# Kernel tuning notes

Measured on AMD Instinct MI355X. Metric: run time of the kernel, lower is better.

Reference implementation:

```python
import jax, jax.numpy as jnp
import numpy as np

B, L, E = 4096, 50, 128


def setup_inputs() -> dict:
    key = jax.random.key(0)
    ks = jax.random.split(key, 12)
    s = 1.0 / np.sqrt(E)
    return {
        "A": jax.random.uniform(ks[0], (B, L, 2 * L), dtype=jnp.float32),
        "hidden": jax.random.normal(ks[1], (B, L, E), dtype=jnp.float32),
        "w_ih": jax.random.normal(ks[2], (3 * E, 2 * E), dtype=jnp.float32) * s,
        "w_hh": jax.random.normal(ks[3], (3 * E, E), dtype=jnp.float32) * s,
        "b_ih": jax.random.normal(ks[4], (3 * E,), dtype=jnp.float32) * s,
        "b_hh": jax.random.normal(ks[5], (3 * E,), dtype=jnp.float32) * s,
        "b_iah": jax.random.normal(ks[6], (E,), dtype=jnp.float32) * s,
        "b_ioh": jax.random.normal(ks[7], (E,), dtype=jnp.float32) * s,
        "w_in": jax.random.normal(ks[8], (E, E), dtype=jnp.float32) * s,
        "b_in": jax.random.normal(ks[9], (E,), dtype=jnp.float32) * s,
        "w_out": jax.random.normal(ks[10], (E, E), dtype=jnp.float32) * s,
        "b_out": jax.random.normal(ks[11], (E,), dtype=jnp.float32) * s,
    }


STEP = 1


def _gnn_cell(A, hidden, w_ih, w_hh, b_ih, b_hh, b_iah, b_ioh, w_in, b_in, w_out, b_out):
    L_ = A.shape[1]
    # linear_edge_in / linear_edge_out (torch Linear: x @ W.T + b)
    h_in = jnp.einsum('ble,fe->blf', hidden, w_in) + b_in
    h_out = jnp.einsum('ble,fe->blf', hidden, w_out) + b_out
    # adjacency propagation: A = [A_in | A_out] along last dim
    input_in = jnp.matmul(A[:, :, :L_], h_in) + b_iah     # [B,L,E]
    input_out = jnp.matmul(A[:, :, L_:2 * L_], h_out) + b_ioh
    inputs = jnp.concatenate([input_in, input_out], axis=2)  # [B,L,2E]
    gi = jnp.einsum('blf,gf->blg', inputs, w_ih) + b_ih      # [B,L,3E]
    gh = jnp.einsum('ble,ge->blg', hidden, w_hh) + b_hh      # [B,L,3E]
    i_r, i_i, i_n = jnp.split(gi, 3, axis=2)
    h_r, h_i, h_n = jnp.split(gh, 3, axis=2)
    reset_gate = jax.nn.sigmoid(i_r + h_r)
    input_gate = jax.nn.sigmoid(i_i + h_i)
    new_gate = jnp.tanh(i_n + reset_gate * h_n)
    return (1 - input_gate) * hidden + input_gate * new_gate


def reference(A, hidden, w_ih, w_hh, b_ih, b_hh, b_iah, b_ioh, w_in, b_in, w_out, b_out):
    for _ in range(STEP):
        hidden = _gnn_cell(A, hidden, w_ih, w_hh, b_ih, b_hh, b_iah, b_ioh, w_in, b_in, w_out, b_out)
    return hidden
```

## Files before the change

kernel.cpp:

```cpp
#include <hip/hip_runtime.h>


using f32x4 = __attribute__((ext_vector_type(4))) float;
using s16x8 = __attribute__((ext_vector_type(8))) short;
using u32x2 = __attribute__((ext_vector_type(2))) unsigned;

#define MFMA(a, b, c) __builtin_amdgcn_mfma_f32_16x16x32_bf16((a), (b), (c), 0, 0, 0)

__device__ __forceinline__ unsigned short f2bf(float x) {
    unsigned u = __float_as_uint(x);
    u += 0x7fffu + ((u >> 16) & 1u);
    return (unsigned short)(u >> 16);
}
__device__ __forceinline__ float bf2f(unsigned short b) {
    return __uint_as_float(((unsigned)b) << 16);
}
__device__ __forceinline__ unsigned pkbf(float a, float b) {
    unsigned r;
    asm("v_cvt_pk_bf16_f32 %0, %1, %2" : "=v"(r) : "v"(a), "v"(b));
    return r;
}

__global__ void wconv_kernel(const float* __restrict__ w_in, const float* __restrict__ w_out,
                             const float* __restrict__ w_hh, const float* __restrict__ w_ih,
                             unsigned short* __restrict__ W1, unsigned short* __restrict__ Wih) {
    int i = blockIdx.x * 256 + threadIdx.x;
    if (i < 81920) {
        float v = (i < 16384) ? w_in[i] : (i < 32768) ? w_out[i - 16384] : w_hh[i - 32768];
        W1[i] = f2bf(v);
    } else if (i < 180224) {
        int j = i - 81920;
        Wih[j] = f2bf(w_ih[j]);
    }
}

#define LDS_BYTES 125952

__launch_bounds__(512, 1)
__global__ void gnn_kernel(const float* __restrict__ A, const float* __restrict__ H,
                           const unsigned short* __restrict__ W1, const unsigned short* __restrict__ Wih,
                           const float* __restrict__ b_ih, const float* __restrict__ b_hh,
                           const float* __restrict__ b_iah, const float* __restrict__ b_ioh,
                           const float* __restrict__ b_in, const float* __restrict__ b_out,
                           float* __restrict__ out) {
    extern __shared__ char smem[];
    unsigned short* sHhi = (unsigned short*)(smem + 0);
    unsigned short* sHlo = (unsigned short*)(smem + 17408);
    unsigned short* sAhi = (unsigned short*)(smem + 34816);
    unsigned short* sThi = (unsigned short*)(smem + 52224);
    unsigned short* sTlo = (unsigned short*)(smem + 89088);
    unsigned short* sIhi = (unsigned short*)(smem + 52224);
    unsigned short* sIlo = (unsigned short*)(smem + 86016);

    const int b    = blockIdx.x;
    const int tid  = threadIdx.x;
    const int wv   = tid >> 6;
    const int lane = tid & 63;
    const int l16  = lane & 15;
    const int l4   = lane >> 4;

    const float* Hb = H + (size_t)b * 6400;
    const float* Ab = A + (size_t)b * 5000;

    s16x8 w1f[4][5];
    #pragma unroll
    for (int kt = 0; kt < 4; ++kt)
        #pragma unroll
        for (int t = 0; t < 5; ++t)
            w1f[kt][t] = *(const s16x8*)(W1 + ((wv + 8 * t) * 16 + l16) * 128 + kt * 32 + l4 * 8);

    {
        const float4* H4 = (const float4*)Hb;
        #pragma unroll
        for (int i = 0; i < 4; ++i) {
            int idx = i * 512 + tid;
            if (idx < 1600) {
                int r = idx >> 5, c = (idx & 31) * 4;
                float4 v = H4[idx];
                unsigned h01 = pkbf(v.x, v.y), h23 = pkbf(v.z, v.w);
                float g0 = __uint_as_float(h01 << 16), g1 = __uint_as_float(h01 & 0xffff0000u);
                float g2 = __uint_as_float(h23 << 16), g3 = __uint_as_float(h23 & 0xffff0000u);
                unsigned l01 = pkbf(v.x - g0, v.y - g1), l23 = pkbf(v.z - g2, v.w - g3);
                u32x2 vh; vh[0] = h01; vh[1] = h23;
                u32x2 vl; vl[0] = l01; vl[1] = l23;
                *(u32x2*)(sHhi + r * 136 + c) = vh;
                *(u32x2*)(sHlo + r * 136 + c) = vl;
            }
        }
        #pragma unroll
        for (int i = 0; i < 4; ++i) {
            int idx = i * 512 + tid;
            if (idx < 1792) {
                int pl = idx >= 896 ? 1 : 0;
                int j = idx - pl * 896;
                int r = 50 + (j >> 6), c = (j & 63) * 2;
                *(unsigned*)((pl ? sHlo : sHhi) + r * 136 + c) = 0u;
            }
        }
        const float2* A2 = (const float2*)Ab;
        #pragma unroll
        for (int i = 0; i < 5; ++i) {
            int idx = i * 512 + tid;
            if (idx < 2500) {
                int r = idx / 50, j = idx - r * 50;
                float2 v = A2[idx];
                int dc = (j < 25) ? (2 * j) : (2 * j + 14);
                *(unsigned*)(sAhi + r * 136 + dc) = pkbf(v.x, v.y);
            }
        }
        #pragma unroll
        for (int i = 0; i < 4; ++i) {
            int idx = i * 512 + tid;
            if (idx < 1596) {
                int r, c;
                if (idx < 700) {
                    r = idx / 14; int k = idx - r * 14;
                    c = (k < 7) ? (50 + 2 * k) : (100 + 2 * k);
                } else {
                    int j = idx - 700;
                    r = 50 + (j >> 6); c = (j & 63) * 2;
                }
                *(unsigned*)(sAhi + r * 136 + c) = 0u;
            }
        }
    }
    __syncthreads();

    const f32x4 vzero = {0.f, 0.f, 0.f, 0.f};

    f32x4 acc_io[2][4];
    f32x4 acc_gh[3][4];
    #pragma unroll
    for (int t = 0; t < 2; ++t)
        #pragma unroll
        for (int m = 0; m < 4; ++m) acc_io[t][m] = vzero;
    #pragma unroll
    for (int t = 0; t < 3; ++t)
        #pragma unroll
        for (int m = 0; m < 4; ++m) acc_gh[t][m] = vzero;

    s16x8 ah[2][4], al[2][4];
    #pragma unroll
    for (int mt = 0; mt < 4; ++mt) {
        int off = (mt * 16 + l16) * 136 + l4 * 8;
        ah[0][mt] = *(const s16x8*)(sHhi + off);
        al[0][mt] = *(const s16x8*)(sHlo + off);
    }
    #pragma unroll
    for (int kt = 0; kt < 4; ++kt) {
        const int cur = kt & 1, nxt = cur ^ 1;
        if (kt < 3) {
            #pragma unroll
            for (int mt = 0; mt < 4; ++mt) {
                int off = (mt * 16 + l16) * 136 + (kt + 1) * 32 + l4 * 8;
                ah[nxt][mt] = *(const s16x8*)(sHhi + off);
                al[nxt][mt] = *(const s16x8*)(sHlo + off);
            }
        }
        #pragma unroll
        for (int t = 0; t < 5; ++t)
            #pragma unroll
            for (int mt = 0; mt < 4; ++mt) {
                if (t < 2) {
                    f32x4 a = acc_io[t][mt];
                    a = MFMA(ah[cur][mt], w1f[kt][t], a);
                    a = MFMA(al[cur][mt], w1f[kt][t], a);
                    acc_io[t][mt] = a;
                } else {
                    f32x4 a = acc_gh[t - 2][mt];
                    a = MFMA(ah[cur][mt], w1f[kt][t], a);
                    a = MFMA(al[cur][mt], w1f[kt][t], a);
                    acc_gh[t - 2][mt] = a;
                }
            }
    }

    s16x8 wihf[8][3];
    #pragma unroll
    for (int kt = 0; kt < 8; ++kt)
        #pragma unroll
        for (int t = 0; t < 3; ++t)
            wihf[kt][t] = *(const s16x8*)(Wih + ((wv + 8 * t) * 16 + l16) * 256 + kt * 32 + l4 * 8);

    #pragma unroll
    for (int t = 0; t < 2; ++t) {
        int n = (wv + 8 * t) * 16 + l16;
        float bias = (n < 128) ? b_in[n] : b_out[n - 128];
        #pragma unroll
        for (int mt = 0; mt < 4; ++mt) {
            int mb = mt * 16 + l4 * 4;
            float x0 = acc_io[t][mt][0] + bias, x1 = acc_io[t][mt][1] + bias;
            float x2 = acc_io[t][mt][2] + bias, x3 = acc_io[t][mt][3] + bias;
            unsigned h01 = pkbf(x0, x1), h23 = pkbf(x2, x3);
            float g0 = __uint_as_float(h01 << 16), g1 = __uint_as_float(h01 & 0xffff0000u);
            float g2 = __uint_as_float(h23 << 16), g3 = __uint_as_float(h23 & 0xffff0000u);
            unsigned l01 = pkbf(x0 - g0, x1 - g1), l23 = pkbf(x2 - g2, x3 - g3);
            u32x2 vh; vh[0] = h01; vh[1] = h23;
            u32x2 vl; vl[0] = l01; vl[1] = l23;
            *(u32x2*)(sThi + n * 72 + mb) = vh;
            *(u32x2*)(sTlo + n * 72 + mb) = vl;
        }
    }
    __syncthreads();

    const int p = wv >> 2, q = wv & 3;
    f32x4 acc2[2][4];
    #pragma unroll
    for (int t = 0; t < 2; ++t)
        #pragma unroll
        for (int m = 0; m < 4; ++m) acc2[t][m] = vzero;

    {
        s16x8 a2[2][4], th2[2][2], tl2[2][2];
        #pragma unroll
        for (int kt = 0; kt < 2; ++kt) {
            #pragma unroll
            for (int mt = 0; mt < 4; ++mt)
                a2[kt][mt] = *(const s16x8*)(sAhi + (mt * 16 + l16) * 136 + p * 64 + kt * 32 + l4 * 8);
            #pragma unroll
            for (int t = 0; t < 2; ++t) {
                int hr = p * 128 + (q + 4 * t) * 16 + l16;
                th2[kt][t] = *(const s16x8*)(sThi + hr * 72 + kt * 32 + l4 * 8);
                tl2[kt][t] = *(const s16x8*)(sTlo + hr * 72 + kt * 32 + l4 * 8);
            }
        }
        #pragma unroll
        for (int kt = 0; kt < 2; ++kt)
            #pragma unroll
            for (int t = 0; t < 2; ++t)
                #pragma unroll
                for (int mt = 0; mt < 4; ++mt) {
                    f32x4 a = acc2[t][mt];
                    a = MFMA(a2[kt][mt], th2[kt][t], a);
                    a = MFMA(a2[kt][mt], tl2[kt][t], a);
                    acc2[t][mt] = a;
                }
    }
    __syncthreads();
    #pragma unroll
    for (int t = 0; t < 2; ++t) {
        int n = p * 128 + (q + 4 * t) * 16 + l16;
        float bias = (n < 128) ? b_iah[n] : b_ioh[n - 128];
        #pragma unroll
        for (int mt = 0; mt < 4; ++mt) {
            int mb = mt * 16 + l4 * 4;
            #pragma unroll
            for (int rr = 0; rr < 4; rr += 2) {
                float x0 = acc2[t][mt][rr] + bias, x1 = acc2[t][mt][rr + 1] + bias;
                unsigned h = pkbf(x0, x1);
                float g0 = __uint_as_float(h << 16), g1 = __uint_as_float(h & 0xffff0000u);
                unsigned l = pkbf(x0 - g0, x1 - g1);
                sIhi[(mb + rr) * 264 + n]     = (unsigned short)(h & 0xffffu);
                sIhi[(mb + rr + 1) * 264 + n] = (unsigned short)(h >> 16);
                sIlo[(mb + rr) * 264 + n]     = (unsigned short)(l & 0xffffu);
                sIlo[(mb + rr + 1) * 264 + n] = (unsigned short)(l >> 16);
            }
        }
    }
    __syncthreads();

    f32x4 acc_n[4];
    #pragma unroll
    for (int m = 0; m < 4; ++m) acc_n[m] = vzero;

    #pragma unroll
    for (int mt = 0; mt < 4; ++mt) {
        int off = (mt * 16 + l16) * 264 + l4 * 8;
        ah[0][mt] = *(const s16x8*)(sIhi + off);
        al[0][mt] = *(const s16x8*)(sIlo + off);
    }
    #pragma unroll
    for (int kt = 0; kt < 8; ++kt) {
        const int cur = kt & 1, nxt = cur ^ 1;
        if (kt < 7) {
            #pragma unroll
            for (int mt = 0; mt < 4; ++mt) {
                int off = (mt * 16 + l16) * 264 + (kt + 1) * 32 + l4 * 8;
                ah[nxt][mt] = *(const s16x8*)(sIhi + off);
                al[nxt][mt] = *(const s16x8*)(sIlo + off);
            }
        }
        #pragma unroll
        for (int t = 0; t < 3; ++t)
            #pragma unroll
            for (int mt = 0; mt < 4; ++mt) {
                if (t < 2) {
                    f32x4 a = acc_gh[t][mt];
                    a = MFMA(ah[cur][mt], wihf[kt][t], a);
                    a = MFMA(al[cur][mt], wihf[kt][t], a);
                    acc_gh[t][mt] = a;
                } else {
                    f32x4 a = acc_n[mt];
                    a = MFMA(ah[cur][mt], wihf[kt][t], a);
                    a = MFMA(al[cur][mt], wihf[kt][t], a);
                    acc_n[mt] = a;
                }
            }
    }

    {
        const int e = wv * 16 + l16;
        const float br   = b_ih[e]       + b_hh[e];
        const float bi   = b_ih[128 + e] + b_hh[128 + e];
        const float bn_i = b_ih[256 + e];
        const float bn_h = b_hh[256 + e];
        float* Ob = out + (size_t)b * 6400;
        #pragma unroll
        for (int mt = 0; mt < 4; ++mt) {
            #pragma unroll
            for (int r = 0; r < 4; ++r) {
                int m = mt * 16 + l4 * 4 + r;
                if (m < 50) {
                    float argr = acc_gh[0][mt][r] + br;
                    float argi = acc_gh[1][mt][r] + bi;
                    float i_n  = acc_n[mt][r] + bn_i;
                    float h_n  = acc_gh[2][mt][r] + bn_h;
                    float rg = 1.f / (1.f + __expf(-argr));
                    float ig = 1.f / (1.f + __expf(-argi));
                    float ta = i_n + rg * h_n;
                    ta = fminf(fmaxf(ta, -30.f), 30.f);
                    float ex = __expf(2.f * ta);
                    float ng = (ex - 1.f) / (ex + 1.f);
                    float h0 = bf2f(sHhi[m * 136 + e]) + bf2f(sHlo[m * 136 + e]);
                    Ob[m * 128 + e] = h0 + ig * (ng - h0);
                }
            }
        }
    }
}

extern "C" void kernel_launch(void* const* d_in, const int* in_sizes, int n_in,
                              void* d_out, int out_size, void* d_ws, size_t ws_size,
                              hipStream_t stream) {
    const float* A     = (const float*)d_in[0];
    const float* hidden= (const float*)d_in[1];
    const float* w_ih  = (const float*)d_in[2];
    const float* w_hh  = (const float*)d_in[3];
    const float* b_ih  = (const float*)d_in[4];
    const float* b_hh  = (const float*)d_in[5];
    const float* b_iah = (const float*)d_in[6];
    const float* b_ioh = (const float*)d_in[7];
    const float* w_in  = (const float*)d_in[8];
    const float* b_in  = (const float*)d_in[9];
    const float* w_out = (const float*)d_in[10];
    const float* b_out = (const float*)d_in[11];
    float* out = (float*)d_out;

    unsigned short* W1  = (unsigned short*)d_ws;
    unsigned short* Wih = W1 + 81920;

    wconv_kernel<<<704, 256, 0, stream>>>(w_in, w_out, w_hh, w_ih, W1, Wih);

    const int nbatch = in_sizes[1] / 6400;
    (void)hipFuncSetAttribute((const void*)gnn_kernel,
                              hipFuncAttributeMaxDynamicSharedMemorySize, LDS_BYTES);
    gnn_kernel<<<nbatch, 512, LDS_BYTES, stream>>>(A, hidden, W1, Wih,
                                                   b_ih, b_hh, b_iah, b_ioh,
                                                   b_in, b_out, out);
}
```

Before: 542.4 us.

## Make blocks persistent over 16 batches with register prefetch of next inputs

Each block now loops over 16 consecutive batch elements instead of handling one. The LDS padding zeroing is done once per block. The next element's H and A are loaded into registers while the current one is computed, so global load latency overlaps with MFMA work. The cost is that the grid shrinks from 4096 to 256 blocks, which roughly matches the CU count at one block per CU, so per-CU latency hiding now depends on the prefetch. Weight fragments are still reloaded every iteration, and the extra prefetch registers raise register pressure.

```diff
diff --git a/kernel.cpp b/kernel.cpp
--- a/kernel.cpp
+++ b/kernel.cpp
@@ -3,6 +3,7 @@
 
 using f32x4 = __attribute__((ext_vector_type(4))) float;
 using s16x8 = __attribute__((ext_vector_type(8))) short;
+using s16x4 = __attribute__((ext_vector_type(4))) short;
 using u32x2 = __attribute__((ext_vector_type(2))) unsigned;
 
 #define MFMA(a, b, c) __builtin_amdgcn_mfma_f32_16x16x32_bf16((a), (b), (c), 0, 0, 0)
@@ -42,7 +43,7 @@
                            const float* __restrict__ b_ih, const float* __restrict__ b_hh,
                            const float* __restrict__ b_iah, const float* __restrict__ b_ioh,
                            const float* __restrict__ b_in, const float* __restrict__ b_out,
-                           float* __restrict__ out) {
+                           float* __restrict__ out, int nbatch) {
     extern __shared__ char smem[];
     unsigned short* sHhi = (unsigned short*)(smem + 0);
     unsigned short* sHlo = (unsigned short*)(smem + 17408);
@@ -52,35 +53,75 @@
     unsigned short* sIhi = (unsigned short*)(smem + 52224);
     unsigned short* sIlo = (unsigned short*)(smem + 86016);
 
-    const int b    = blockIdx.x;
     const int tid  = threadIdx.x;
     const int wv   = tid >> 6;
     const int lane = tid & 63;
     const int l16  = lane & 15;
     const int l4   = lane >> 4;
 
-    const float* Hb = H + (size_t)b * 6400;
-    const float* Ab = A + (size_t)b * 5000;
-
-    s16x8 w1f[4][5];
     #pragma unroll
-    for (int kt = 0; kt < 4; ++kt)
-        #pragma unroll
-        for (int t = 0; t < 5; ++t)
-            w1f[kt][t] = *(const s16x8*)(W1 + ((wv + 8 * t) * 16 + l16) * 128 + kt * 32 + l4 * 8);
-
+    for (int i = 0; i < 4; ++i) {
+        int idx = i * 512 + tid;
+        if (idx < 1792) {
+            int pl = idx >= 896 ? 1 : 0;
+            int j = idx - pl * 896;
+            int r = 50 + (j >> 6), c = (j & 63) * 2;
+            *(unsigned*)((pl ? sHlo : sHhi) + r * 136 + c) = 0u;
+        }
+    }
+    #pragma unroll
+    for (int i = 0; i < 4; ++i) {
+        int idx = i * 512 + tid;
+        if (idx < 1596) {
+            int r, c;
+            if (idx < 700) {
+                r = idx / 14; int k = idx - r * 14;
+                c = (k < 7) ? (50 + 2 * k) : (100 + 2 * k);
+            } else {
+                int j = idx - 700;
+                r = 50 + (j >> 6); c = (j & 63) * 2;
+            }
+            *(unsigned*)(sAhi + r * 136 + c) = 0u;
+        }
+    }
+
+    const int g0 = blockIdx.x * 16;
+    const int ng = (nbatch - g0 < 16) ? (nbatch - g0) : 16;
+
+    float4 hreg[4];
+    float2 areg[5];
     {
-        const float4* H4 = (const float4*)Hb;
+        const float4* H4 = (const float4*)(H + (size_t)g0 * 6400);
+        const float2* A2 = (const float2*)(A + (size_t)g0 * 5000);
+        #pragma unroll
+        for (int i = 0; i < 4; ++i) { int idx = i * 512 + tid; if (idx < 1600) hreg[i] = H4[idx]; }
+        #pragma unroll
+        for (int i = 0; i < 5; ++i) { int idx = i * 512 + tid; if (idx < 2500) areg[i] = A2[idx]; }
+    }
+
+    const f32x4 vzero = {0.f, 0.f, 0.f, 0.f};
+
+    #pragma unroll 1
+    for (int it = 0; it < ng; ++it) {
+        const int g = g0 + it;
+
+        s16x8 w1f[4][5];
+        #pragma unroll
+        for (int kt = 0; kt < 4; ++kt)
+            #pragma unroll
+            for (int t = 0; t < 5; ++t)
+                w1f[kt][t] = *(const s16x8*)(W1 + ((wv + 8 * t) * 16 + l16) * 128 + kt * 32 + l4 * 8);
+
         #pragma unroll
         for (int i = 0; i < 4; ++i) {
             int idx = i * 512 + tid;
             if (idx < 1600) {
                 int r = idx >> 5, c = (idx & 31) * 4;
-                float4 v = H4[idx];
+                float4 v = hreg[i];
                 unsigned h01 = pkbf(v.x, v.y), h23 = pkbf(v.z, v.w);
-                float g0 = __uint_as_float(h01 << 16), g1 = __uint_as_float(h01 & 0xffff0000u);
-                float g2 = __uint_as_float(h23 << 16), g3 = __uint_as_float(h23 & 0xffff0000u);
-                unsigned l01 = pkbf(v.x - g0, v.y - g1), l23 = pkbf(v.z - g2, v.w - g3);
+                float g0f = __uint_as_float(h01 << 16), g1f = __uint_as_float(h01 & 0xffff0000u);
+                float g2f = __uint_as_float(h23 << 16), g3f = __uint_as_float(h23 & 0xffff0000u);
+                unsigned l01 = pkbf(v.x - g0f, v.y - g1f), l23 = pkbf(v.z - g2f, v.w - g3f);
                 u32x2 vh; vh[0] = h01; vh[1] = h23;
                 u32x2 vl; vl[0] = l01; vl[1] = l23;
                 *(u32x2*)(sHhi + r * 136 + c) = vh;
@@ -88,244 +129,226 @@
             }
         }
         #pragma unroll
-        for (int i = 0; i < 4; ++i) {
-            int idx = i * 512 + tid;
-            if (idx < 1792) {
-                int pl = idx >= 896 ? 1 : 0;
-                int j = idx - pl * 896;
-                int r = 50 + (j >> 6), c = (j & 63) * 2;
-                *(unsigned*)((pl ? sHlo : sHhi) + r * 136 + c) = 0u;
-            }
-        }
-        const float2* A2 = (const float2*)Ab;
-        #pragma unroll
         for (int i = 0; i < 5; ++i) {
             int idx = i * 512 + tid;
             if (idx < 2500) {
                 int r = idx / 50, j = idx - r * 50;
-                float2 v = A2[idx];
+                float2 v = areg[i];
                 int dc = (j < 25) ? (2 * j) : (2 * j + 14);
                 *(unsigned*)(sAhi + r * 136 + dc) = pkbf(v.x, v.y);
             }
         }
-        #pragma unroll
-        for (int i = 0; i < 4; ++i) {
-            int idx = i * 512 + tid;
-            if (idx < 1596) {
-                int r, c;
-                if (idx < 700) {
-                    r = idx / 14; int k = idx - r * 14;
-                    c = (k < 7) ? (50 + 2 * k) : (100 + 2 * k);
-                } else {
-                    int j = idx - 700;
-                    r = 50 + (j >> 6); c = (j & 63) * 2;
-                }
-                *(unsigned*)(sAhi + r * 136 + c) = 0u;
-            }
-        }
-    }
-    __syncthreads();
-
-    const f32x4 vzero = {0.f, 0.f, 0.f, 0.f};
-
-    f32x4 acc_io[2][4];
-    f32x4 acc_gh[3][4];
-    #pragma unroll
-    for (int t = 0; t < 2; ++t)
-        #pragma unroll
-        for (int m = 0; m < 4; ++m) acc_io[t][m] = vzero;
-    #pragma unroll
-    for (int t = 0; t < 3; ++t)
-        #pragma unroll
-        for (int m = 0; m < 4; ++m) acc_gh[t][m] = vzero;
-
-    s16x8 ah[2][4], al[2][4];
-    #pragma unroll
-    for (int mt = 0; mt < 4; ++mt) {
-        int off = (mt * 16 + l16) * 136 + l4 * 8;
-        ah[0][mt] = *(const s16x8*)(sHhi + off);
-        al[0][mt] = *(const s16x8*)(sHlo + off);
-    }
-    #pragma unroll
-    for (int kt = 0; kt < 4; ++kt) {
-        const int cur = kt & 1, nxt = cur ^ 1;
-        if (kt < 3) {
+
+        if (it + 1 < ng) {
+            const float4* H4 = (const float4*)(H + (size_t)(g + 1) * 6400);
+            const float2* A2 = (const float2*)(A + (size_t)(g + 1) * 5000);
+            #pragma unroll
+            for (int i = 0; i < 4; ++i) { int idx = i * 512 + tid; if (idx < 1600) hreg[i] = H4[idx]; }
+            #pragma unroll
+            for (int i = 0; i < 5; ++i) { int idx = i * 512 + tid; if (idx < 2500) areg[i] = A2[idx]; }
+        }
+        __syncthreads();
+
+        f32x4 acc_io[2][4];
+        f32x4 acc_gh[3][4];
+        #pragma unroll
+        for (int t = 0; t < 2; ++t)
+            #pragma unroll
+            for (int m = 0; m < 4; ++m) acc_io[t][m] = vzero;
+        #pragma unroll
+        for (int t = 0; t < 3; ++t)
+            #pragma unroll
+            for (int m = 0; m < 4; ++m) acc_gh[t][m] = vzero;
+
+        s16x8 ah[2][4], al[2][4];
+        #pragma unroll
+        for (int mt = 0; mt < 4; ++mt) {
+            int off = (mt * 16 + l16) * 136 + l4 * 8;
+            ah[0][mt] = *(const s16x8*)(sHhi + off);
+            al[0][mt] = *(const s16x8*)(sHlo + off);
+        }
+        #pragma unroll
+        for (int kt = 0; kt < 4; ++kt) {
+            const int cur = kt & 1, nxt = cur ^ 1;
+            if (kt < 3) {
+                #pragma unroll
+                for (int mt = 0; mt < 4; ++mt) {
+                    int off = (mt * 16 + l16) * 136 + (kt + 1) * 32 + l4 * 8;
+                    ah[nxt][mt] = *(const s16x8*)(sHhi + off);
+                    al[nxt][mt] = *(const s16x8*)(sHlo + off);
+                }
+            }
+            #pragma unroll
+            for (int t = 0; t < 5; ++t)
+                #pragma unroll
+                for (int mt = 0; mt < 4; ++mt) {
+                    if (t < 2) {
+                        f32x4 a = acc_io[t][mt];
+                        a = MFMA(ah[cur][mt], w1f[kt][t], a);
+                        a = MFMA(al[cur][mt], w1f[kt][t], a);
+                        acc_io[t][mt] = a;
+                    } else {
+                        f32x4 a = acc_gh[t - 2][mt];
+                        a = MFMA(ah[cur][mt], w1f[kt][t], a);
+                        a = MFMA(al[cur][mt], w1f[kt][t], a);
+                        acc_gh[t - 2][mt] = a;
+                    }
+                }
+        }
+
+        s16x8 wihf[8][3];
+        #pragma unroll
+        for (int kt = 0; kt < 8; ++kt)
+            #pragma unroll
+            for (int t = 0; t < 3; ++t)
+                wihf[kt][t] = *(const s16x8*)(Wih + ((wv + 8 * t) * 16 + l16) * 256 + kt * 32 + l4 * 8);
+
+        #pragma unroll
+        for (int t = 0; t < 2; ++t) {
+            int n = (wv + 8 * t) * 16 + l16;
+            float bias = (n < 128) ? b_in[n] : b_out[n - 128];
             #pragma unroll
             for (int mt = 0; mt < 4; ++mt) {
-                int off = (mt * 16 + l16) * 136 + (kt + 1) * 32 + l4 * 8;
-                ah[nxt][mt] = *(const s16x8*)(sHhi + off);
-                al[nxt][mt] = *(const s16x8*)(sHlo + off);
-            }
-        }
-        #pragma unroll
-        for (int t = 0; t < 5; ++t)
+                int mb = mt * 16 + l4 * 4;
+                float x0 = acc_io[t][mt][0] + bias, x1 = acc_io[t][mt][1] + bias;
+                float x2 = acc_io[t][mt][2] + bias, x3 = acc_io[t][mt][3] + bias;
+                unsigned h01 = pkbf(x0, x1), h23 = pkbf(x2, x3);
+                float q0 = __uint_as_float(h01 << 16), q1 = __uint_as_float(h01 & 0xffff0000u);
+                float q2 = __uint_as_float(h23 << 16), q3 = __uint_as_float(h23 & 0xffff0000u);
+                unsigned l01 = pkbf(x0 - q0, x1 - q1), l23 = pkbf(x2 - q2, x3 - q3);
+                u32x2 vh; vh[0] = h01; vh[1] = h23;
+                u32x2 vl; vl[0] = l01; vl[1] = l23;
+                *(u32x2*)(sThi + n * 72 + mb) = vh;
+                *(u32x2*)(sTlo + n * 72 + mb) = vl;
+            }
+        }
+        __syncthreads();
+
+        const int p = wv >> 2, q = wv & 3;
+        f32x4 acc2[2][4];
+        #pragma unroll
+        for (int t = 0; t < 2; ++t)
+            #pragma unroll
+            for (int m = 0; m < 4; ++m) acc2[t][m] = vzero;
+
+        {
+            s16x8 a2[2][4], th2[2][2], tl2[2][2];
+            #pragma unroll
+            for (int kt = 0; kt < 2; ++kt) {
+                #pragma unroll
+                for (int mt = 0; mt < 4; ++mt)
+                    a2[kt][mt] = *(const s16x8*)(sAhi + (mt * 16 + l16) * 136 + p * 64 + kt * 32 + l4 * 8);
+                #pragma unroll
+                for (int t = 0; t < 2; ++t) {
+                    int hr = p * 128 + (q + 4 * t) * 16 + l16;
+                    th2[kt][t] = *(const s16x8*)(sThi + hr * 72 + kt * 32 + l4 * 8);
+                    tl2[kt][t] = *(const s16x8*)(sTlo + hr * 72 + kt * 32 + l4 * 8);
+                }
+            }
+            #pragma unroll
+            for (int kt = 0; kt < 2; ++kt)
+                #pragma unroll
+                for (int t = 0; t < 2; ++t)
+                    #pragma unroll
+                    for (int mt = 0; mt < 4; ++mt) {
+                        f32x4 a = acc2[t][mt];
+                        a = MFMA(a2[kt][mt], th2[kt][t], a);
+                        a = MFMA(a2[kt][mt], tl2[kt][t], a);
+                        acc2[t][mt] = a;
+                    }
+        }
+        __syncthreads();
+        #pragma unroll
+        for (int t = 0; t < 2; ++t) {
+            int n = p * 128 + (q + 4 * t) * 16 + l16;
+            float bias = (n < 128) ? b_iah[n] : b_ioh[n - 128];
             #pragma unroll
             for (int mt = 0; mt < 4; ++mt) {
-                if (t < 2) {
-                    f32x4 a = acc_io[t][mt];
-                    a = MFMA(ah[cur][mt], w1f[kt][t], a);
-                    a = MFMA(al[cur][mt], w1f[kt][t], a);
-                    acc_io[t][mt] = a;
-                } else {
-                    f32x4 a = acc_gh[t - 2][mt];
-                    a = MFMA(ah[cur][mt], w1f[kt][t], a);
-                    a = MFMA(al[cur][mt], w1f[kt][t], a);
-                    acc_gh[t - 2][mt] = a;
-                }
-            }
-    }
-
-    s16x8 wihf[8][3];
-    #pragma unroll
-    for (int kt = 0; kt < 8; ++kt)
-        #pragma unroll
-        for (int t = 0; t < 3; ++t)
-            wihf[kt][t] = *(const s16x8*)(Wih + ((wv + 8 * t) * 16 + l16) * 256 + kt * 32 + l4 * 8);
-
-    #pragma unroll
-    for (int t = 0; t < 2; ++t) {
-        int n = (wv + 8 * t) * 16 + l16;
-        float bias = (n < 128) ? b_in[n] : b_out[n - 128];
+                int mb = mt * 16 + l4 * 4;
+                #pragma unroll
+                for (int rr = 0; rr < 4; rr += 2) {
+                    float x0 = acc2[t][mt][rr] + bias, x1 = acc2[t][mt][rr + 1] + bias;
+                    unsigned h = pkbf(x0, x1);
+                    float q0 = __uint_as_float(h << 16), q1 = __uint_as_float(h & 0xffff0000u);
+                    unsigned l = pkbf(x0 - q0, x1 - q1);
+                    sIhi[(mb + rr) * 264 + n]     = (unsigned short)(h & 0xffffu);
+                    sIhi[(mb + rr + 1) * 264 + n] = (unsigned short)(h >> 16);
+                    sIlo[(mb + rr) * 264 + n]     = (unsigned short)(l & 0xffffu);
+                    sIlo[(mb + rr + 1) * 264 + n] = (unsigned short)(l >> 16);
+                }
+            }
+        }
+        __syncthreads();
+
+        f32x4 acc_n[4];
+        #pragma unroll
+        for (int m = 0; m < 4; ++m) acc_n[m] = vzero;
+
         #pragma unroll
         for (int mt = 0; mt < 4; ++mt) {
-            int mb = mt * 16 + l4 * 4;
-            float x0 = acc_io[t][mt][0] + bias, x1 = acc_io[t][mt][1] + bias;
-            float x2 = acc_io[t][mt][2] + bias, x3 = acc_io[t][mt][3] + bias;
-            unsigned h01 = pkbf(x0, x1), h23 = pkbf(x2, x3);
-            float g0 = __uint_as_float(h01 << 16), g1 = __uint_as_float(h01 & 0xffff0000u);
-            float g2 = __uint_as_float(h23 << 16), g3 = __uint_as_float(h23 & 0xffff0000u);
-            unsigned l01 = pkbf(x0 - g0, x1 - g1), l23 = pkbf(x2 - g2, x3 - g3);
-            u32x2 vh; vh[0] = h01; vh[1] = h23;
-            u32x2 vl; vl[0] = l01; vl[1] = l23;
-            *(u32x2*)(sThi + n * 72 + mb) = vh;
-            *(u32x2*)(sTlo + n * 72 + mb) = vl;
-        }
-    }
-    __syncthreads();
-
-    const int p = wv >> 2, q = wv & 3;
-    f32x4 acc2[2][4];
-    #pragma unroll
-    for (int t = 0; t < 2; ++t)
-        #pragma unroll
-        for (int m = 0; m < 4; ++m) acc2[t][m] = vzero;
-
-    {
-        s16x8 a2[2][4], th2[2][2], tl2[2][2];
-        #pragma unroll
-        for (int kt = 0; kt < 2; ++kt) {
-            #pragma unroll
-            for (int mt = 0; mt < 4; ++mt)
-                a2[kt][mt] = *(const s16x8*)(sAhi + (mt * 16 + l16) * 136 + p * 64 + kt * 32 + l4 * 8);
-            #pragma unroll
-            for (int t = 0; t < 2; ++t) {
-                int hr = p * 128 + (q + 4 * t) * 16 + l16;
-                th2[kt][t] = *(const s16x8*)(sThi + hr * 72 + kt * 32 + l4 * 8);
-                tl2[kt][t] = *(const s16x8*)(sTlo + hr * 72 + kt * 32 + l4 * 8);
-            }
-        }
-        #pragma unroll
-        for (int kt = 0; kt < 2; ++kt)
-            #pragma unroll
-            for (int t = 0; t < 2; ++t)
+            int off = (mt * 16 + l16) * 264 + l4 * 8;
+            ah[0][mt] = *(const s16x8*)(sIhi + off);
+            al[0][mt] = *(const s16x8*)(sIlo + off);
+        }
+        #pragma unroll
+        for (int kt = 0; kt < 8; ++kt) {
+            const int cur = kt & 1, nxt = cur ^ 1;
+            if (kt < 7) {
                 #pragma unroll
                 for (int mt = 0; mt < 4; ++mt) {
-                    f32x4 a = acc2[t][mt];
-                    a = MFMA(a2[kt][mt], th2[kt][t], a);
-                    a = MFMA(a2[kt][mt], tl2[kt][t], a);
-                    acc2[t][mt] = a;
-                }
-    }
-    __syncthreads();
-    #pragma unroll
-    for (int t = 0; t < 2; ++t) {
-        int n = p * 128 + (q + 4 * t) * 16 + l16;
-        float bias = (n < 128) ? b_iah[n] : b_ioh[n - 128];
-        #pragma unroll
-        for (int mt = 0; mt < 4; ++mt) {
-            int mb = mt * 16 + l4 * 4;
-            #pragma unroll
-            for (int rr = 0; rr < 4; rr += 2) {
-                float x0 = acc2[t][mt][rr] + bias, x1 = acc2[t][mt][rr + 1] + bias;
-                unsigned h = pkbf(x0, x1);
-                float g0 = __uint_as_float(h << 16), g1 = __uint_as_float(h & 0xffff0000u);
-                unsigned l = pkbf(x0 - g0, x1 - g1);
-                sIhi[(mb + rr) * 264 + n]     = (unsigned short)(h & 0xffffu);
-                sIhi[(mb + rr + 1) * 264 + n] = (unsigned short)(h >> 16);
-                sIlo[(mb + rr) * 264 + n]     = (unsigned short)(l & 0xffffu);
-                sIlo[(mb + rr + 1) * 264 + n] = (unsigned short)(l >> 16);
-            }
-        }
-    }
-    __syncthreads();
-
-    f32x4 acc_n[4];
-    #pragma unroll
-    for (int m = 0; m < 4; ++m) acc_n[m] = vzero;
-
-    #pragma unroll
-    for (int mt = 0; mt < 4; ++mt) {
-        int off = (mt * 16 + l16) * 264 + l4 * 8;
-        ah[0][mt] = *(const s16x8*)(sIhi + off);
-        al[0][mt] = *(const s16x8*)(sIlo + off);
-    }
-    #pragma unroll
-    for (int kt = 0; kt < 8; ++kt) {
-        const int cur = kt & 1, nxt = cur ^ 1;
-        if (kt < 7) {
+                    int off = (mt * 16 + l16) * 264 + (kt + 1) * 32 + l4 * 8;
+                    ah[nxt][mt] = *(const s16x8*)(sIhi + off);
+                    al[nxt][mt] = *(const s16x8*)(sIlo + off);
+                }
+            }
+            #pragma unroll
+            for (int t = 0; t < 3; ++t)
+                #pragma unroll
+                for (int mt = 0; mt < 4; ++mt) {
+                    if (t < 2) {
+                        f32x4 a = acc_gh[t][mt];
+                        a = MFMA(ah[cur][mt], wihf[kt][t], a);
+                        a = MFMA(al[cur][mt], wihf[kt][t], a);
+                        acc_gh[t][mt] = a;
+                    } else {
+                        f32x4 a = acc_n[mt];
+                        a = MFMA(ah[cur][mt], wihf[kt][t], a);
+                        a = MFMA(al[cur][mt], wihf[kt][t], a);
+                        acc_n[mt] = a;
+                    }
+                }
+        }
+
+        {
+            const int e = wv * 16 + l16;
+            const float br   = b_ih[e]       + b_hh[e];
+            const float bi   = b_ih[128 + e] + b_hh[128 + e];
+            const float bn_i = b_ih[256 + e];
+            const float bn_h = b_hh[256 + e];
+            float* Ob = out + (size_t)g * 6400;
             #pragma unroll
             for (int mt = 0; mt < 4; ++mt) {
-                int off = (mt * 16 + l16) * 264 + (kt + 1) * 32 + l4 * 8;
-                ah[nxt][mt] = *(const s16x8*)(sIhi + off);
-                al[nxt][mt] = *(const s16x8*)(sIlo + off);
-            }
-        }
-        #pragma unroll
-        for (int t = 0; t < 3; ++t)
-            #pragma unroll
-            for (int mt = 0; mt < 4; ++mt) {
-                if (t < 2) {
-                    f32x4 a = acc_gh[t][mt];
-                    a = MFMA(ah[cur][mt], wihf[kt][t], a);
-                    a = MFMA(al[cur][mt], wihf[kt][t], a);
-                    acc_gh[t][mt] = a;
-                } else {
-                    f32x4 a = acc_n[mt];
-                    a = MFMA(ah[cur][mt], wihf[kt][t], a);
-                    a = MFMA(al[cur][mt], wihf[kt][t], a);
-                    acc_n[mt] = a;
-                }
-            }
-    }
-
-    {
-        const int e = wv * 16 + l16;
-        const float br   = b_ih[e]       + b_hh[e];
-        const float bi   = b_ih[128 + e] + b_hh[128 + e];
-        const float bn_i = b_ih[256 + e];
-        const float bn_h = b_hh[256 + e];
-        float* Ob = out + (size_t)b * 6400;
-        #pragma unroll
-        for (int mt = 0; mt < 4; ++mt) {
-            #pragma unroll
-            for (int r = 0; r < 4; ++r) {
-                int m = mt * 16 + l4 * 4 + r;
-                if (m < 50) {
-                    float argr = acc_gh[0][mt][r] + br;
-                    float argi = acc_gh[1][mt][r] + bi;
-                    float i_n  = acc_n[mt][r] + bn_i;
-                    float h_n  = acc_gh[2][mt][r] + bn_h;
-                    float rg = 1.f / (1.f + __expf(-argr));
-                    float ig = 1.f / (1.f + __expf(-argi));
-                    float ta = i_n + rg * h_n;
-                    ta = fminf(fmaxf(ta, -30.f), 30.f);
-                    float ex = __expf(2.f * ta);
-                    float ng = (ex - 1.f) / (ex + 1.f);
-                    float h0 = bf2f(sHhi[m * 136 + e]) + bf2f(sHlo[m * 136 + e]);
-                    Ob[m * 128 + e] = h0 + ig * (ng - h0);
-                }
-            }
-        }
+                #pragma unroll
+                for (int r = 0; r < 4; ++r) {
+                    int m = mt * 16 + l4 * 4 + r;
+                    if (m < 50) {
+                        float argr = acc_gh[0][mt][r] + br;
+                        float argi = acc_gh[1][mt][r] + bi;
+                        float i_n  = acc_n[mt][r] + bn_i;
+                        float h_n  = acc_gh[2][mt][r] + bn_h;
+                        float rg = 1.f / (1.f + __expf(-argr));
+                        float ig = 1.f / (1.f + __expf(-argi));
+                        float ta = i_n + rg * h_n;
+                        ta = fminf(fmaxf(ta, -30.f), 30.f);
+                        float ex = __expf(2.f * ta);
+                        float ng2 = (ex - 1.f) / (ex + 1.f);
+                        float h0 = bf2f(sHhi[m * 136 + e]) + bf2f(sHlo[m * 136 + e]);
+                        Ob[m * 128 + e] = h0 + ig * (ng2 - h0);
+                    }
+                }
+            }
+        }
+        __syncthreads();
     }
 }
 
@@ -352,9 +375,10 @@
     wconv_kernel<<<704, 256, 0, stream>>>(w_in, w_out, w_hh, w_ih, W1, Wih);
 
     const int nbatch = in_sizes[1] / 6400;
+    const int nblk   = (nbatch + 15) / 16;
     (void)hipFuncSetAttribute((const void*)gnn_kernel,
                               hipFuncAttributeMaxDynamicSharedMemorySize, LDS_BYTES);
-    gnn_kernel<<<nbatch, 512, LDS_BYTES, stream>>>(A, hidden, W1, Wih,
-                                                   b_ih, b_hh, b_iah, b_ioh,
-                                                   b_in, b_out, out);
-}
+    gnn_kernel<<<nblk, 512, LDS_BYTES, stream>>>(A, hidden, W1, Wih,
+                                                 b_ih, b_hh, b_iah, b_ioh,
+                                                 b_in, b_out, out, nbatch);
+}
```

New measurement: 1.240 ms. 2.29x slower.
